# Kernel optimization log

Measured on AMD Instinct MI355X. Metric: run time of the kernel, lower is better.

Reference implementation:

```python
import jax, jax.numpy as jnp
import numpy as np

T_SIZE = 64
S_SIZE = 256
NUM_HEADS = 12
DEPTH = 12
DIM = 768
MLP_DIM = 3072
EPS = 1e-5
BATCH = 32
N_TOK = 2 * T_SIZE + S_SIZE  # 384


def setup_inputs() -> dict:
    key = jax.random.key(0)
    ks = jax.random.split(key, 6)
    s = 0.02
    return {
        "x": jax.random.normal(ks[0], (BATCH, N_TOK, DIM), jnp.float32),
        "qkv_w": jax.random.normal(ks[1], (DEPTH, DIM, 3 * DIM), jnp.float32) * s,
        "qkv_b": jnp.zeros((DEPTH, 3 * DIM), jnp.float32),
        "proj_w": jax.random.normal(ks[2], (DEPTH, DIM, DIM), jnp.float32) * s,
        "proj_b": jnp.zeros((DEPTH, DIM), jnp.float32),
        "ln1_g": jnp.ones((DEPTH, DIM), jnp.float32),
        "ln1_b": jnp.zeros((DEPTH, DIM), jnp.float32),
        "ln2_g": jnp.ones((DEPTH, DIM), jnp.float32),
        "ln2_b": jnp.zeros((DEPTH, DIM), jnp.float32),
        "fc1_w": jax.random.normal(ks[3], (DEPTH, DIM, MLP_DIM), jnp.float32) * s,
        "fc1_b": jnp.zeros((DEPTH, MLP_DIM), jnp.float32),
        "fc2_w": jax.random.normal(ks[4], (DEPTH, MLP_DIM, DIM), jnp.float32) * s,
        "fc2_b": jnp.zeros((DEPTH, DIM), jnp.float32),
    }


def _layernorm(x, g, b):
    m = jnp.mean(x, axis=-1, keepdims=True)
    v = jnp.mean((x - m) ** 2, axis=-1, keepdims=True)
    return (x - m) * jax.lax.rsqrt(v + EPS) * g + b


def _attention(x, wqkv, bqkv, wp, bp):
    B, N, C = x.shape
    hd = C // NUM_HEADS
    scale = hd ** -0.5
    # [B,N,3C] -> [3,B,H,N,hd]
    qkv = (x @ wqkv + bqkv).reshape(B, N, 3, NUM_HEADS, hd).transpose(2, 0, 3, 1, 4)
    q, k, v = qkv[0], qkv[1], qkv[2]
    q_t = q[:, :, :T_SIZE]
    q_it = q[:, :, T_SIZE:2 * T_SIZE]
    q_s = q[:, :, 2 * T_SIZE:]
    k_it = k[:, :, T_SIZE:2 * T_SIZE]
    v_it = v[:, :, T_SIZE:2 * T_SIZE]
    # mix attention: (t, s) queries over ALL keys
    q_ts = jnp.concatenate([q_t, q_s], axis=2)  # [B,H,t+s,hd]
    mix = jax.nn.softmax(jnp.einsum('bhqd,bhkd->bhqk', q_ts, k) * scale, axis=-1)
    ts = jnp.einsum('bhqk,bhkd->bhqd', mix, v).transpose(0, 2, 1, 3).reshape(B, T_SIZE + S_SIZE, C)
    # inherent attention: it queries over it keys only
    inh = jax.nn.softmax(jnp.einsum('bhqd,bhkd->bhqk', q_it, k_it) * scale, axis=-1)
    it = jnp.einsum('bhqk,bhkd->bhqd', inh, v_it).transpose(0, 2, 1, 3).reshape(B, T_SIZE, C)
    out = jnp.concatenate([ts[:, :T_SIZE], it, ts[:, T_SIZE:]], axis=1)
    return out @ wp + bp


def reference(x, qkv_w, qkv_b, proj_w, proj_b, ln1_g, ln1_b, ln2_g, ln2_b,
              fc1_w, fc1_b, fc2_w, fc2_b):
    for l in range(DEPTH):
        x = x + _attention(_layernorm(x, ln1_g[l], ln1_b[l]),
                           qkv_w[l], qkv_b[l], proj_w[l], proj_b[l])
        h = _layernorm(x, ln2_g[l], ln2_b[l])
        h = jax.nn.gelu(h @ fc1_w[l] + fc1_b[l], approximate=False)
        x = x + (h @ fc2_w[l] + fc2_b[l])
    return x
```

## Files before the change

kernel.cpp:

```cpp
#include <hip/hip_runtime.h>
#include <cstdint>

typedef unsigned short u16;
typedef __attribute__((ext_vector_type(8))) short bf16x8;
typedef __attribute__((ext_vector_type(4))) float f32x4;

#define B_SZ 32
#define NTOK 384
#define DIM 768
#define NH 12
#define HD 64
#define MLP 3072
#define MROWS (B_SZ * NTOK)

__device__ __forceinline__ float b2f(u16 h) { return __uint_as_float(((unsigned)h) << 16); }
__device__ __forceinline__ u16 f2b(float f) {
    unsigned u = __float_as_uint(f);
    unsigned r = u + 0x7fffu + ((u >> 16) & 1u);
    return (u16)(r >> 16);
}

__device__ __forceinline__ void load_lds16(const void* g, void* l) {
    __builtin_amdgcn_global_load_lds(
        (const __attribute__((address_space(1))) unsigned*)g,
        (__attribute__((address_space(3))) unsigned*)l, 16, 0, 0);
}

__device__ __forceinline__ float gelu_fast(float v) {
    float u2 = -1.5957691216f * v * (1.0f + 0.044715f * v * v);
    return v * __builtin_amdgcn_rcpf(1.0f + __expf(u2));
}

__global__ void detect_kernel(const u16* __restrict__ x, int* __restrict__ flagp) {
    __shared__ int cnt;
    if (threadIdx.x == 0) cnt = 0;
    __syncthreads();
    int bad = 0;
    for (int i = threadIdx.x; i < 4096; i += 256) {
        int e = (x[i] >> 7) & 0xFF;
        if (e >= 0xC0) bad++;
    }
    atomicAdd(&cnt, bad);
    __syncthreads();
    if (threadIdx.x == 0) *flagp = (cnt > 4) ? 1 : 0;
}

__global__ void conv_any(const void* __restrict__ src, u16* __restrict__ dst, int n,
                         const int* __restrict__ flagp) {
    int i = blockIdx.x * 256 + threadIdx.x;
    if (i >= n) return;
    dst[i] = (*flagp) ? f2b(((const float*)src)[i]) : ((const u16*)src)[i];
}

__global__ void load_x(const void* __restrict__ src, float* __restrict__ dst, int n,
                       const int* __restrict__ flagp) {
    int i = blockIdx.x * 256 + threadIdx.x;
    if (i >= n) return;
    dst[i] = (*flagp) ? ((const float*)src)[i] : b2f(((const u16*)src)[i]);
}

__global__ void store_out(const float* __restrict__ src, void* __restrict__ dst, int n,
                          const int* __restrict__ flagp) {
    int i = blockIdx.x * 256 + threadIdx.x;
    if (i >= n) return;
    if (*flagp) ((float*)dst)[i] = src[i];
    else ((u16*)dst)[i] = f2b(src[i]);
}

__global__ __launch_bounds__(256) void transpose_k(const void* __restrict__ in, size_t ioff,
                                                   u16* __restrict__ outp, int K, int N,
                                                   const int* __restrict__ flagp) {
    __shared__ u16 t[32][33];
    const int flag = *flagp;
    const int n0 = blockIdx.x << 5, k0 = blockIdx.y << 5;
    const int tx = threadIdx.x, ty = threadIdx.y;
#pragma unroll
    for (int i = 0; i < 4; i++) {
        size_t idx = ioff + (size_t)(k0 + ty + i * 8) * N + n0 + tx;
        t[ty + i * 8][tx] = flag ? f2b(((const float*)in)[idx]) : ((const u16*)in)[idx];
    }
    __syncthreads();
#pragma unroll
    for (int i = 0; i < 4; i++)
        outp[(size_t)(n0 + ty + i * 8) * K + k0 + tx] = t[tx][ty + i * 8];
}

template <int MODE, int TM>
__global__ __launch_bounds__(256) void gemm_bt(const u16* __restrict__ A,
                                               const u16* __restrict__ Bt,
                                               const u16* __restrict__ bias,
                                               u16* __restrict__ outb,
                                               float* __restrict__ outf,
                                               int N, int K) {
    constexpr int MI = (TM == 128) ? 4 : 2;
    constexpr int AT = (TM == 128) ? 4 : 2;
    __shared__ u16 lA[TM * 64];
    __shared__ u16 lB[128 * 64];
    const int tid = threadIdx.x;
    const int wave = tid >> 6, lane = tid & 63;
    const int quad = lane >> 4, l16 = lane & 15;

    const int gx = gridDim.x;
    const int nwg = gx * gridDim.y;
    const int orig = blockIdx.y * gx + blockIdx.x;
    const int xcd = orig & 7, loc = orig >> 3;
    const int qq = nwg >> 3, rr = nwg & 7;
    const int wgid = (xcd < rr ? xcd * (qq + 1) : rr * (qq + 1) + (xcd - rr) * qq) + loc;
    const int bx = wgid % gx, by = wgid / gx;

    const int m0 = by * TM, n0 = bx << 7;
    const int wm = (wave & 1) * (TM / 2), wn = (wave >> 1) << 6;
    const int lr = lane >> 3;
    const int swz = ((lane & 7) ^ lr) << 3;

    f32x4 acc[MI][4] = {};

    const u16* gA = A + (size_t)(m0 + wave * (8 * AT) + lr) * K + swz;
    const u16* gB = Bt + (size_t)(n0 + wave * 32 + lr) * K + swz;

    for (int kt = 0; kt < K; kt += 64) {
        __syncthreads();
#pragma unroll
        for (int t = 0; t < AT; t++)
            load_lds16(gA + kt + (size_t)t * 8 * K, &lA[(wave * AT + t) * 512 + lane * 8]);
#pragma unroll
        for (int t = 0; t < 4; t++)
            load_lds16(gB + kt + (size_t)t * 8 * K, &lB[(wave * 4 + t) * 512 + lane * 8]);
        __syncthreads();
        const int xs = l16 & 7;
#pragma unroll
        for (int kk = 0; kk < 2; kk++) {
            bf16x8 af[MI], bfr[4];
            const int ksel = ((kk << 2) + quad);
#pragma unroll
            for (int i = 0; i < MI; i++)
                af[i] = *(const bf16x8*)&lA[(wm + i * 16 + l16) * 64 + ((ksel ^ xs) << 3)];
#pragma unroll
            for (int j = 0; j < 4; j++)
                bfr[j] = *(const bf16x8*)&lB[(wn + j * 16 + l16) * 64 + ((ksel ^ xs) << 3)];
#pragma unroll
            for (int i = 0; i < MI; i++)
#pragma unroll
                for (int j = 0; j < 4; j++)
                    acc[i][j] = __builtin_amdgcn_mfma_f32_16x16x32_bf16(af[i], bfr[j], acc[i][j], 0, 0, 0);
        }
    }

#pragma unroll
    for (int j = 0; j < 4; j++) {
        const int n = n0 + wn + j * 16 + l16;
        const float bv = b2f(bias[n]);
#pragma unroll
        for (int i = 0; i < MI; i++) {
            const int mrow = m0 + wm + i * 16 + quad * 4;
#pragma unroll
            for (int r = 0; r < 4; r++) {
                float v = acc[i][j][r] + bv;
                size_t idx = (size_t)(mrow + r) * N + n;
                if (MODE == 0) {
                    outb[idx] = f2b(v);
                } else if (MODE == 1) {
                    outb[idx] = f2b(gelu_fast(v));
                } else {
                    outf[idx] += v;
                }
            }
        }
    }
}

__global__ __launch_bounds__(256) void ln_kernel(const float* __restrict__ x,
                                                 const u16* __restrict__ g,
                                                 const u16* __restrict__ bta,
                                                 u16* __restrict__ y) {
    const int wave = threadIdx.x >> 6, lane = threadIdx.x & 63;
    const int row = (blockIdx.x << 2) + wave;
    const float4* xr = (const float4*)(x + (size_t)row * DIM);
    float4 v[3];
    float s = 0.f, sq = 0.f;
#pragma unroll
    for (int i = 0; i < 3; i++) {
        v[i] = xr[i * 64 + lane];
        s += v[i].x + v[i].y + v[i].z + v[i].w;
        sq += v[i].x * v[i].x + v[i].y * v[i].y + v[i].z * v[i].z + v[i].w * v[i].w;
    }
#pragma unroll
    for (int off = 32; off >= 1; off >>= 1) {
        s += __shfl_xor(s, off, 64);
        sq += __shfl_xor(sq, off, 64);
    }
    const float mean = s * (1.f / DIM);
    const float var = sq * (1.f / DIM) - mean * mean;
    const float rs = rsqrtf(var + 1e-5f);
    u16* yr = y + (size_t)row * DIM;
#pragma unroll
    for (int i = 0; i < 3; i++) {
        ushort4 gg = ((const ushort4*)g)[i * 64 + lane];
        ushort4 bb = ((const ushort4*)bta)[i * 64 + lane];
        ushort4 o;
        o.x = f2b((v[i].x - mean) * rs * b2f(gg.x) + b2f(bb.x));
        o.y = f2b((v[i].y - mean) * rs * b2f(gg.y) + b2f(bb.y));
        o.z = f2b((v[i].z - mean) * rs * b2f(gg.z) + b2f(bb.z));
        o.w = f2b((v[i].w - mean) * rs * b2f(gg.w) + b2f(bb.w));
        ((ushort4*)yr)[i * 64 + lane] = o;
    }
}

template <int NJ, int JLO>
__global__ __launch_bounds__(256) void attn_kernel(const u16* __restrict__ qkv,
                                                   u16* __restrict__ out) {
    __shared__ u16 vT[64 * 392];
    __shared__ u16 pbuf[4][16 * 72];
    const int bx = blockIdx.x;
    const int qt = (NJ == 24) ? (bx + (bx >= 1 ? 1 : 0)) : 1;
    const int h = blockIdx.y, b = blockIdx.z;
    const int tid = threadIdx.x, wave = tid >> 6, lane = tid & 63;
    const int quad = lane >> 4, l16 = lane & 15;
    const u16* base = qkv + (size_t)b * NTOK * (3 * DIM);

    for (int it = tid; it < NTOK * 8; it += 256) {
        const int key = it >> 3, dseg = it & 7;
        const u16* gp = base + (size_t)key * (3 * DIM) + 2 * DIM + h * HD + dseg * 8;
        ushort4 u0 = ((const ushort4*)gp)[0];
        ushort4 u1 = ((const ushort4*)gp)[1];
        u16 vals[8] = {u0.x, u0.y, u0.z, u0.w, u1.x, u1.y, u1.z, u1.w};
#pragma unroll
        for (int t = 0; t < 8; t++) {
            const int i = (t + key) & 7;
            vT[(dseg * 8 + i) * 392 + key] = vals[i];
        }
    }

    bf16x8 qf[2];
    const int qrow = qt * 64 + wave * 16 + l16;
#pragma unroll
    for (int s = 0; s < 2; s++)
        qf[s] = *(const bf16x8*)(base + (size_t)qrow * (3 * DIM) + h * HD + s * 32 + quad * 8);

    __syncthreads();

    f32x4 sacc[NJ];
#pragma unroll
    for (int j = 0; j < NJ; j++) {
        const int key = (JLO + j) * 16 + l16;
        const u16* kb = base + (size_t)key * (3 * DIM) + DIM + h * HD;
        bf16x8 k0 = *(const bf16x8*)(kb + quad * 8);
        bf16x8 k1 = *(const bf16x8*)(kb + 32 + quad * 8);
        f32x4 z = {0.f, 0.f, 0.f, 0.f};
        z = __builtin_amdgcn_mfma_f32_16x16x32_bf16(qf[0], k0, z, 0, 0, 0);
        sacc[j] = __builtin_amdgcn_mfma_f32_16x16x32_bf16(qf[1], k1, z, 0, 0, 0);
    }

    float mx[4] = {-1e30f, -1e30f, -1e30f, -1e30f};
#pragma unroll
    for (int j = 0; j < NJ; j++)
#pragma unroll
        for (int r = 0; r < 4; r++) mx[r] = fmaxf(mx[r], sacc[j][r]);
#pragma unroll
    for (int off = 1; off < 16; off <<= 1)
#pragma unroll
        for (int r = 0; r < 4; r++) mx[r] = fmaxf(mx[r], __shfl_xor(mx[r], off, 64));

    float sm[4] = {0.f, 0.f, 0.f, 0.f};
#pragma unroll
    for (int j = 0; j < NJ; j++)
#pragma unroll
        for (int r = 0; r < 4; r++) {
            float e = __expf((sacc[j][r] - mx[r]) * 0.125f);
            sacc[j][r] = e;
            sm[r] += e;
        }
#pragma unroll
    for (int off = 1; off < 16; off <<= 1)
#pragma unroll
        for (int r = 0; r < 4; r++) sm[r] += __shfl_xor(sm[r], off, 64);
    float inv[4];
#pragma unroll
    for (int r = 0; r < 4; r++) inv[r] = 1.f / sm[r];

    f32x4 oacc[4] = {};
    u16* pb = &pbuf[wave][0];
#pragma unroll
    for (int c = 0; c < NJ / 4; c++) {
        __syncthreads();
#pragma unroll
        for (int jj = 0; jj < 4; jj++) {
#pragma unroll
            for (int r = 0; r < 4; r++)
                pb[(quad * 4 + r) * 72 + jj * 16 + l16] = f2b(sacc[c * 4 + jj][r] * inv[r]);
        }
        __syncthreads();
#pragma unroll
        for (int s = 0; s < 2; s++) {
            bf16x8 pf = *(const bf16x8*)&pb[l16 * 72 + s * 32 + quad * 8];
            const int kcol = JLO * 16 + c * 64 + s * 32 + quad * 8;
#pragma unroll
            for (int jd = 0; jd < 4; jd++) {
                bf16x8 vf = *(const bf16x8*)&vT[(jd * 16 + l16) * 392 + kcol];
                oacc[jd] = __builtin_amdgcn_mfma_f32_16x16x32_bf16(pf, vf, oacc[jd], 0, 0, 0);
            }
        }
    }

    const int q = qt * 64 + wave * 16 + quad * 4;
    u16* orow = out + (size_t)(b * NTOK + q) * DIM + h * HD;
#pragma unroll
    for (int jd = 0; jd < 4; jd++)
#pragma unroll
        for (int r = 0; r < 4; r++)
            orow[(size_t)r * DIM + jd * 16 + l16] = f2b(oacc[jd][r]);
}

extern "C" void kernel_launch(void* const* d_in, const int* in_sizes, int n_in,
                              void* d_out, int out_size, void* d_ws, size_t ws_size,
                              hipStream_t stream) {
    const void* x_in   = d_in[0];
    const void* qkv_w  = d_in[1];
    const void* qkv_b  = d_in[2];
    const void* proj_w = d_in[3];
    const void* proj_b = d_in[4];
    const void* ln1_g  = d_in[5];
    const void* ln1_b  = d_in[6];
    const void* ln2_g  = d_in[7];
    const void* ln2_b  = d_in[8];
    const void* fc1_w  = d_in[9];
    const void* fc1_b  = d_in[10];
    const void* fc2_w  = d_in[11];
    const void* fc2_b  = d_in[12];

    constexpr size_t SZ_X32 = (size_t)MROWS * DIM * 4;
    constexpr size_t SZ_ABUF = (size_t)MROWS * DIM * 2;
    constexpr size_t SZ_BIG = (size_t)MROWS * MLP * 2;
    constexpr size_t SZ_WT = (size_t)(2304 * 768 + 768 * 768 + 3072 * 768 + 768 * 3072) * 2;
    constexpr size_t SZ_PAR = 262144;
    const size_t fixed = SZ_X32 + SZ_ABUF + SZ_WT + SZ_PAR + 256;

    int nc;
    if (fixed + SZ_BIG <= ws_size) nc = 1;
    else if (fixed + SZ_BIG / 2 <= ws_size) nc = 2;
    else nc = 4;
    const size_t bigsz = SZ_BIG / nc;

    char* ws = (char*)d_ws;
    float* x32 = (float*)ws;
    u16* abuf = (u16*)(ws + SZ_X32);
    u16* big = (u16*)(ws + SZ_X32 + SZ_ABUF);
    u16* wqt = (u16*)(ws + SZ_X32 + SZ_ABUF + bigsz);
    u16* wpt = wqt + 2304 * 768;
    u16* w1t = wpt + 768 * 768;
    u16* w2t = w1t + 3072 * 768;
    u16* par = w2t + 768 * 3072;
    int* flagp = (int*)((char*)(par) + SZ_PAR);

    u16* p_qkvb = par;
    u16* p_projb = p_qkvb + 12 * 2304;
    u16* p_ln1g = p_projb + 12 * 768;
    u16* p_ln1b = p_ln1g + 12 * 768;
    u16* p_ln2g = p_ln1b + 12 * 768;
    u16* p_ln2b = p_ln2g + 12 * 768;
    u16* p_fc1b = p_ln2b + 12 * 768;
    u16* p_fc2b = p_fc1b + 12 * 3072;

    const int NEL = MROWS * DIM;
    detect_kernel<<<1, 256, 0, stream>>>((const u16*)x_in, flagp);
    load_x<<<(NEL + 255) / 256, 256, 0, stream>>>(x_in, x32, NEL, flagp);
    conv_any<<<(12 * 2304 + 255) / 256, 256, 0, stream>>>(qkv_b, p_qkvb, 12 * 2304, flagp);
    conv_any<<<(12 * 768 + 255) / 256, 256, 0, stream>>>(proj_b, p_projb, 12 * 768, flagp);
    conv_any<<<(12 * 768 + 255) / 256, 256, 0, stream>>>(ln1_g, p_ln1g, 12 * 768, flagp);
    conv_any<<<(12 * 768 + 255) / 256, 256, 0, stream>>>(ln1_b, p_ln1b, 12 * 768, flagp);
    conv_any<<<(12 * 768 + 255) / 256, 256, 0, stream>>>(ln2_g, p_ln2g, 12 * 768, flagp);
    conv_any<<<(12 * 768 + 255) / 256, 256, 0, stream>>>(ln2_b, p_ln2b, 12 * 768, flagp);
    conv_any<<<(12 * 3072 + 255) / 256, 256, 0, stream>>>(fc1_b, p_fc1b, 12 * 3072, flagp);
    conv_any<<<(12 * 768 + 255) / 256, 256, 0, stream>>>(fc2_b, p_fc2b, 12 * 768, flagp);

    const int CR = MROWS / nc;
    const int CB = B_SZ / nc;

    for (int l = 0; l < 12; l++) {
        transpose_k<<<dim3(2304 / 32, 768 / 32), dim3(32, 8), 0, stream>>>(
            qkv_w, (size_t)l * DIM * 2304, wqt, DIM, 2304, flagp);
        transpose_k<<<dim3(768 / 32, 768 / 32), dim3(32, 8), 0, stream>>>(
            proj_w, (size_t)l * DIM * DIM, wpt, DIM, DIM, flagp);
        transpose_k<<<dim3(3072 / 32, 768 / 32), dim3(32, 8), 0, stream>>>(
            fc1_w, (size_t)l * DIM * MLP, w1t, DIM, MLP, flagp);
        transpose_k<<<dim3(768 / 32, 3072 / 32), dim3(32, 8), 0, stream>>>(
            fc2_w, (size_t)l * MLP * DIM, w2t, MLP, DIM, flagp);

        for (int c = 0; c < nc; c++) {
            const size_t r0 = (size_t)c * CR;
            ln_kernel<<<CR / 4, 256, 0, stream>>>(x32 + r0 * DIM, p_ln1g + l * DIM,
                                                  p_ln1b + l * DIM, abuf + r0 * DIM);
            gemm_bt<0, 128><<<dim3(2304 / 128, CR / 128), 256, 0, stream>>>(
                abuf + r0 * DIM, wqt, p_qkvb + l * 2304, big, nullptr, 2304, DIM);
            attn_kernel<24, 0><<<dim3(5, NH, CB), 256, 0, stream>>>(big, abuf + r0 * DIM);
            attn_kernel<4, 4><<<dim3(1, NH, CB), 256, 0, stream>>>(big, abuf + r0 * DIM);
            gemm_bt<2, 64><<<dim3(DIM / 128, CR / 64), 256, 0, stream>>>(
                abuf + r0 * DIM, wpt, p_projb + l * DIM, nullptr, x32 + r0 * DIM, DIM, DIM);
        }
        for (int c = 0; c < nc; c++) {
            const size_t r0 = (size_t)c * CR;
            ln_kernel<<<CR / 4, 256, 0, stream>>>(x32 + r0 * DIM, p_ln2g + l * DIM,
                                                  p_ln2b + l * DIM, abuf + r0 * DIM);
            gemm_bt<1, 128><<<dim3(MLP / 128, CR / 128), 256, 0, stream>>>(
                abuf + r0 * DIM, w1t, p_fc1b + l * MLP, big, nullptr, MLP, DIM);
            gemm_bt<2, 64><<<dim3(DIM / 128, CR / 64), 256, 0, stream>>>(
                big, w2t, p_fc2b + l * DIM, nullptr, x32 + r0 * DIM, DIM, MLP);
        }
    }
    store_out<<<(NEL + 255) / 256, 256, 0, stream>>>(x32, d_out, NEL, flagp);
}
```

Baseline: 5.383 ms.

## Remap attention blocks per XCD, trim V staging, drop block barriers

For the mixed-attention launch, the block index is remapped so that all query tiles of one (batch, head) pair land on the same XCD, which should improve L2 reuse of K and V. V is transposed into LDS only for the key range the kernel actually uses, so the inherent-attention kernel no longer stages all 384 keys. The two __syncthreads around each per-wave P buffer are removed because each wave only touches its own buffer. The P buffer row stride changes to 76 to reduce bank conflicts. The catch is that 16-byte LDS reads at a 152-byte row stride are no longer 16-byte aligned, and correctness now depends on ordering within a wave instead of an explicit barrier.

Result: faster. 5.187 ms (-3.6%).

```diff
diff --git a/kernel.cpp b/kernel.cpp
--- a/kernel.cpp
+++ b/kernel.cpp
@@ -209,25 +209,40 @@
 template <int NJ, int JLO>
 __global__ __launch_bounds__(256) void attn_kernel(const u16* __restrict__ qkv,
                                                    u16* __restrict__ out) {
-    __shared__ u16 vT[64 * 392];
-    __shared__ u16 pbuf[4][16 * 72];
-    const int bx = blockIdx.x;
-    const int qt = (NJ == 24) ? (bx + (bx >= 1 ? 1 : 0)) : 1;
-    const int h = blockIdx.y, b = blockIdx.z;
+    constexpr int K0 = JLO * 16;
+    constexpr int NKEY = NJ * 16;
+    constexpr int VSTR = NKEY + 8;
+    __shared__ u16 vT[64 * VSTR];
+    __shared__ u16 pbuf[4][16 * 76];
     const int tid = threadIdx.x, wave = tid >> 6, lane = tid & 63;
     const int quad = lane >> 4, l16 = lane & 15;
+
+    int qt, h, b;
+    if (NJ == 24) {
+        const int id = blockIdx.x + 5 * (blockIdx.y + 12 * blockIdx.z);
+        const int xcd = id & 7, slot = id >> 3;
+        const int ppx = (int)(gridDim.x * gridDim.y * gridDim.z) >> 3;
+        const int s5 = slot / 5;
+        const int pair = xcd * (ppx / 5) + s5;
+        const int qi = slot - 5 * s5;
+        qt = qi + (qi >= 1 ? 1 : 0);
+        h = pair % 12;
+        b = pair / 12;
+    } else {
+        qt = 1; h = blockIdx.y; b = blockIdx.z;
+    }
     const u16* base = qkv + (size_t)b * NTOK * (3 * DIM);
 
-    for (int it = tid; it < NTOK * 8; it += 256) {
-        const int key = it >> 3, dseg = it & 7;
-        const u16* gp = base + (size_t)key * (3 * DIM) + 2 * DIM + h * HD + dseg * 8;
+    for (int it = tid; it < NKEY * 8; it += 256) {
+        const int kk = it >> 3, dseg = it & 7;
+        const u16* gp = base + (size_t)(K0 + kk) * (3 * DIM) + 2 * DIM + h * HD + dseg * 8;
         ushort4 u0 = ((const ushort4*)gp)[0];
         ushort4 u1 = ((const ushort4*)gp)[1];
         u16 vals[8] = {u0.x, u0.y, u0.z, u0.w, u1.x, u1.y, u1.z, u1.w};
 #pragma unroll
         for (int t = 0; t < 8; t++) {
-            const int i = (t + key) & 7;
-            vT[(dseg * 8 + i) * 392 + key] = vals[i];
+            const int i = (t + kk + dseg) & 7;
+            vT[(dseg * 8 + i) * VSTR + kk] = vals[i];
         }
     }
 
@@ -282,21 +297,19 @@
     u16* pb = &pbuf[wave][0];
 #pragma unroll
     for (int c = 0; c < NJ / 4; c++) {
-        __syncthreads();
 #pragma unroll
         for (int jj = 0; jj < 4; jj++) {
 #pragma unroll
             for (int r = 0; r < 4; r++)
-                pb[(quad * 4 + r) * 72 + jj * 16 + l16] = f2b(sacc[c * 4 + jj][r] * inv[r]);
-        }
-        __syncthreads();
+                pb[(quad * 4 + r) * 76 + jj * 16 + l16] = f2b(sacc[c * 4 + jj][r] * inv[r]);
+        }
 #pragma unroll
         for (int s = 0; s < 2; s++) {
-            bf16x8 pf = *(const bf16x8*)&pb[l16 * 72 + s * 32 + quad * 8];
-            const int kcol = JLO * 16 + c * 64 + s * 32 + quad * 8;
+            bf16x8 pf = *(const bf16x8*)&pb[l16 * 76 + s * 32 + quad * 8];
+            const int kc = c * 64 + s * 32 + quad * 8;
 #pragma unroll
             for (int jd = 0; jd < 4; jd++) {
-                bf16x8 vf = *(const bf16x8*)&vT[(jd * 16 + l16) * 392 + kcol];
+                bf16x8 vf = *(const bf16x8*)&vT[(jd * 16 + l16) * VSTR + kc];
                 oacc[jd] = __builtin_amdgcn_mfma_f32_16x16x32_bf16(pf, vf, oacc[jd], 0, 0, 0);
             }
         }
```
